# Kernel tuning notes

Measured on AMD Instinct MI355X. Metric: run time of the kernel, lower is better.

The kernel has to match this reference:

```python
import jax, jax.numpy as jnp
import numpy as np

B_, DIM, HEADS, RES = 2, 288, 12, 32
# per-branch (D_sp, H_sp, W_sp) from idx permutation of split_size=[2,2,4]
WINS = ((2, 2, 4), (2, 2, 4), (2, 4, 2))
POS_DIM = ((DIM // 3) // 4) // 4  # = 6
HB = HEADS // 3  # heads per branch = 4


def _rel_tables(Dsp, Hsp, Wsp):
    d = np.arange(1 - Dsp, Dsp); h = np.arange(1 - Hsp, Hsp); w = np.arange(1 - Wsp, Wsp)
    biases = np.stack(np.meshgrid(d, h, w, indexing='ij')).reshape(3, -1).T.astype(np.float32)
    c = np.stack(np.meshgrid(np.arange(Dsp), np.arange(Hsp), np.arange(Wsp), indexing='ij')).reshape(3, -1)
    rel = (c[:, :, None] - c[:, None, :]).transpose(1, 2, 0).astype(np.int64)
    rel[..., 0] += Dsp - 1; rel[..., 1] += Hsp - 1; rel[..., 2] += Wsp - 1
    rel[..., 0] *= (2 * Hsp - 1) * (2 * Wsp - 1); rel[..., 1] *= 2 * Wsp - 1
    return biases, rel.sum(-1).astype(np.int32)


def _ln(x, g, b):
    m = x.mean(-1, keepdims=True)
    v = jnp.mean((x - m) ** 2, axis=-1, keepdims=True)
    return (x - m) * jax.lax.rsqrt(v + 1e-5) * g + b


def setup_inputs() -> dict:
    key = jax.random.key(0)
    ks = jax.random.split(key, 10)
    C, P, L = DIM, POS_DIM, RES ** 3
    s = 0.02
    x = jax.random.normal(ks[0], (B_, L, C), jnp.float32)
    w_qkv = jax.random.normal(ks[1], (C, 3 * C), jnp.float32) * s
    w_proj = jax.random.normal(ks[2], (C, C), jnp.float32) * s
    b_proj = jnp.zeros((C,), jnp.float32)
    conv_w = jax.random.normal(ks[3], (C, 1, 3, 3, 3), jnp.float32) * s  # depthwise OIDHW
    conv_b = jnp.zeros((C,), jnp.float32)
    pos_proj_w = jax.random.normal(ks[4], (3, 3, P), jnp.float32) * s
    pos_proj_b = jnp.zeros((3, P), jnp.float32)
    ln1_g = jnp.ones((3, P)); ln1_b = jnp.zeros((3, P))
    lin1_w = jax.random.normal(ks[5], (3, P, P), jnp.float32) * s; lin1_b = jnp.zeros((3, P))
    ln2_g = jnp.ones((3, P)); ln2_b = jnp.zeros((3, P))
    lin2_w = jax.random.normal(ks[6], (3, P, P), jnp.float32) * s; lin2_b = jnp.zeros((3, P))
    ln3_g = jnp.ones((3, P)); ln3_b = jnp.zeros((3, P))
    lin3_w = jax.random.normal(ks[7], (3, P, HB), jnp.float32) * s; lin3_b = jnp.zeros((3, HB))
    tabs = [_rel_tables(*w) for w in WINS]
    rpe_biases = jnp.asarray(np.stack([t[0] for t in tabs]))  # (3, 63, 3)
    rel_index = jnp.asarray(np.stack([t[1] for t in tabs]))   # (3, 16, 16)
    return {'x': x, 'D': RES, 'H': RES, 'W': RES, 'w_qkv': w_qkv, 'w_proj': w_proj,
            'b_proj': b_proj, 'conv_w': conv_w, 'conv_b': conv_b,
            'pos_proj_w': pos_proj_w, 'pos_proj_b': pos_proj_b,
            'ln1_g': ln1_g, 'ln1_b': ln1_b, 'lin1_w': lin1_w, 'lin1_b': lin1_b,
            'ln2_g': ln2_g, 'ln2_b': ln2_b, 'lin2_w': lin2_w, 'lin2_b': lin2_b,
            'ln3_g': ln3_g, 'ln3_b': ln3_b, 'lin3_w': lin3_w, 'lin3_b': lin3_b,
            'rpe_biases': rpe_biases, 'rel_index': rel_index}


def reference(x, D, H, W, w_qkv, w_proj, b_proj, conv_w, conv_b,
              pos_proj_w, pos_proj_b, ln1_g, ln1_b, lin1_w, lin1_b,
              ln2_g, ln2_b, lin2_w, lin2_b, ln3_g, ln3_b, lin3_w, lin3_b,
              rpe_biases, rel_index):
    B, L, C = x.shape
    C3 = C // 3
    hd = C3 // HB
    scale = hd ** -0.5
    qkv = (x @ w_qkv).reshape(B, L, 3, C).transpose(2, 0, 1, 3)  # (3, B, L, C)
    outs = []
    for bi, (Dsp, Hsp, Wsp) in enumerate(WINS):
        N = Dsp * Hsp * Wsp
        lo, hi = bi * C3, (bi + 1) * C3

        def to_win(t):
            # (B, L, C3) -> windows (B', HB, N, hd)
            t = t.reshape(B, D // Dsp, Dsp, H // Hsp, Hsp, W // Wsp, Wsp, C3)
            t = t.transpose(0, 1, 3, 5, 2, 4, 6, 7).reshape(-1, N, HB, hd)
            return t.transpose(0, 2, 1, 3)

        q = to_win(qkv[0, :, :, lo:hi]) * scale
        k = to_win(qkv[1, :, :, lo:hi])
        v = to_win(qkv[2, :, :, lo:hi])
        # dynamic relative position bias MLP (residual=False path)
        p = rpe_biases[bi] @ pos_proj_w[bi] + pos_proj_b[bi]
        p = jax.nn.relu(_ln(p, ln1_g[bi], ln1_b[bi])) @ lin1_w[bi] + lin1_b[bi]
        p = jax.nn.relu(_ln(p, ln2_g[bi], ln2_b[bi])) @ lin2_w[bi] + lin2_b[bi]
        p = jax.nn.relu(_ln(p, ln3_g[bi], ln3_b[bi])) @ lin3_w[bi] + lin3_b[bi]  # (T, HB)
        bias = p[rel_index[bi].reshape(-1)].reshape(N, N, HB).transpose(2, 0, 1)  # (HB, N, N)
        attn = jax.nn.softmax(jnp.einsum('whnd,whmd->whnm', q, k) + bias[None], axis=-1)
        o = jnp.einsum('whnm,whmd->whnd', attn, v)
        o = o.transpose(0, 2, 1, 3).reshape(B, D // Dsp, H // Hsp, W // Wsp, Dsp, Hsp, Wsp, C3)
        o = o.transpose(0, 1, 4, 2, 5, 3, 6, 7).reshape(B, D, H, W, C3)
        outs.append(o)
    att = jnp.concatenate(outs, axis=-1).reshape(B, L, C)
    # locally-enhanced branch: depthwise 3x3x3 conv over v
    vimg = qkv[2].reshape(B, D, H, W, C).transpose(0, 4, 1, 2, 3)
    lcm = jax.lax.conv_general_dilated(vimg, conv_w, (1, 1, 1), 'SAME',
                                       dimension_numbers=('NCDHW', 'OIDHW', 'NCDHW'),
                                       feature_group_count=C)
    lcm = (lcm + conv_b[None, :, None, None, None]).transpose(0, 2, 3, 4, 1).reshape(B, L, C)
    return (att + lcm) @ w_proj + b_proj
```

## Files before the change

### kernel.cpp

```cpp
#include <hip/hip_runtime.h>
#include <hip/hip_bf16.h>
#include <math.h>

#define BATCH 2
#define RES   32
#define LTOK  32768
#define CDIM  288
#define NQKV  864
#define MROWS 65536

typedef unsigned short u16;
typedef u16   u16x4 __attribute__((ext_vector_type(4)));
typedef short s16x8 __attribute__((ext_vector_type(8)));
typedef float f32x4 __attribute__((ext_vector_type(4)));

__device__ __forceinline__ u16 f2bf(float f) {
  union { __hip_bfloat16 h; u16 u; } x;
  x.h = __float2bfloat16(f);
  return x.u;
}
__device__ __forceinline__ float bf2f(u16 u) {
  union { u16 u; __hip_bfloat16 h; } x;
  x.u = u;
  return __bfloat162float(x.h);
}
__device__ __forceinline__ float bflo(unsigned u) {
  union { unsigned u; float f; } x; x.u = u << 16; return x.f;
}
__device__ __forceinline__ float bfhi(unsigned u) {
  union { unsigned u; float f; } x; x.u = u & 0xffff0000u; return x.f;
}

#define ASYNC16(gsrc, ldst)                                                        \
  __builtin_amdgcn_global_load_lds(                                                \
      (const __attribute__((address_space(1))) void*)(gsrc),                       \
      (__attribute__((address_space(3))) void*)(ldst), 16, 0, 0)

__global__ __launch_bounds__(256) void transpose_cvt(
    const float* __restrict__ w, u16* __restrict__ wt, int K, int N) {
  int o = blockIdx.x * 256 + threadIdx.x;
  if (o >= N * K) return;
  int n = o / K, k = o - n * K;
  wt[o] = f2bf(w[(size_t)k * N + n]);
}

__global__ __launch_bounds__(256) void conv_w_kmajor(
    const float* __restrict__ cw, float* __restrict__ wck) {
  int o = blockIdx.x * 256 + threadIdx.x;
  if (o >= 27 * 288) return;
  int k = o / 288, c = o - k * 288;
  wck[o] = cw[c * 27 + k];
}

template <bool BF16OUT, bool ABF16>
__global__ __launch_bounds__(512, 2) void gemm_areg(
    const void* __restrict__ Ax, const u16* __restrict__ Bt,
    const float* __restrict__ bias, void* __restrict__ out, int N) {
  __shared__ __align__(16) u16 lds[36864];
  const int bm = blockIdx.x * 128;
  const int tid = threadIdx.x;
  const int lane = tid & 63, wave = tid >> 6;
  const int m16 = lane & 15, kq = lane >> 4;
  const int nf = wave >> 2, mg = wave & 3;
  const int NC = N >> 5;

  if (ABF16) {
    const u16* Ab = (const u16*)Ax;
    for (int i = wave; i < 72; i += 8) {
      int g = i >> 1, rh = i & 1;
      ASYNC16(Ab + (size_t)(bm + rh * 64 + lane) * 288 + g * 8, &lds[i * 512]);
    }
    asm volatile("s_waitcnt vmcnt(0)" ::: "memory");
  } else {
    const float* Af = (const float*)Ax;
#pragma unroll
    for (int p = 0; p < 18; p++) {
      int s = p * 512 + tid;
      int r = s / 72, q = s - r * 72;
      float4 v = *(const float4*)(Af + (size_t)(bm + r) * 288 + q * 4);
      u16x4 pk;
      pk[0] = f2bf(v.x); pk[1] = f2bf(v.y); pk[2] = f2bf(v.z); pk[3] = f2bf(v.w);
      *(u16x4*)&lds[(q >> 1) * 1024 + (r >> 6) * 512 + (r & 63) * 8 + (q & 1) * 4] = pk;
    }
  }
  __syncthreads();

  s16x8 areg[2][9];
#pragma unroll
  for (int j = 0; j < 2; j++) {
    const int row = (mg * 2 + j) * 16 + m16;
    const int base = (row >> 6) * 512 + (row & 63) * 8;
#pragma unroll
    for (int ks = 0; ks < 9; ks++)
      areg[j][ks] = *(const s16x8*)&lds[(ks * 4 + kq) * 1024 + base];
  }
  asm volatile("s_waitcnt lgkmcnt(0)" ::: "memory");
  __builtin_amdgcn_s_barrier();

  {
    const int r = lane & 31, gh = lane >> 5;
    for (int gp = wave; gp < 18; gp += 8)
      ASYNC16(Bt + (size_t)r * 288 + (gp * 2 + gh) * 8, &lds[gp * 512]);
  }
  asm volatile("s_waitcnt vmcnt(0)" ::: "memory");
  __builtin_amdgcn_s_barrier();

  int buf = 0;
  for (int c = 0; c < NC; c++) {
    if (c + 1 < NC) {
      const u16* Bc = Bt + (size_t)(c + 1) * 32 * 288;
      const int r = lane & 31, gh = lane >> 5;
      u16* bb1 = &lds[(buf ^ 1) * 9216];
      for (int gp = wave; gp < 18; gp += 8)
        ASYNC16(Bc + (size_t)r * 288 + (gp * 2 + gh) * 8, &bb1[gp * 512]);
    }
    __builtin_amdgcn_sched_barrier(0);

    const u16* bb = &lds[buf * 9216];
    f32x4 acc0 = {0.f, 0.f, 0.f, 0.f}, acc1 = {0.f, 0.f, 0.f, 0.f};
#pragma unroll
    for (int ks = 0; ks < 9; ks++) {
      s16x8 bf = *(const s16x8*)&bb[(ks * 4 + kq) * 256 + (nf * 16 + m16) * 8];
      acc0 = __builtin_amdgcn_mfma_f32_16x16x32_bf16(areg[0][ks], bf, acc0, 0, 0, 0);
      acc1 = __builtin_amdgcn_mfma_f32_16x16x32_bf16(areg[1][ks], bf, acc1, 0, 0, 0);
    }
    const int col = (c << 5) + nf * 16 + m16;
    const size_t r0 = (size_t)(bm + mg * 32 + kq * 4);
    if (BF16OUT) {
      u16* op = (u16*)out;
#pragma unroll
      for (int r = 0; r < 4; r++) {
        op[(r0 + r) * N + col] = f2bf(acc0[r]);
        op[(r0 + 16 + r) * N + col] = f2bf(acc1[r]);
      }
    } else {
      const float bv = bias ? bias[col] : 0.f;
      float* op = (float*)out;
#pragma unroll
      for (int r = 0; r < 4; r++) {
        op[(r0 + r) * N + col] = acc0[r] + bv;
        op[(r0 + 16 + r) * N + col] = acc1[r] + bv;
      }
    }
    if (c + 1 < NC) {
      asm volatile("s_waitcnt vmcnt(8)" ::: "memory");
      __builtin_amdgcn_s_barrier();
    }
    buf ^= 1;
  }
}

__device__ __forceinline__ void ln_relu6(const float* x, float* o,
                                         const float* g, const float* b) {
  float m = 0.f;
#pragma unroll
  for (int i = 0; i < 6; i++) m += x[i];
  m *= (1.f / 6.f);
  float v = 0.f;
#pragma unroll
  for (int i = 0; i < 6; i++) { float d = x[i] - m; v += d * d; }
  v *= (1.f / 6.f);
  float r = rsqrtf(v + 1e-5f);
#pragma unroll
  for (int i = 0; i < 6; i++) {
    float t = (x[i] - m) * r * g[i] + b[i];
    o[i] = t > 0.f ? t : 0.f;
  }
}

__global__ __launch_bounds__(256) void rpe_mlp(
    const float* __restrict__ rpe, const float* __restrict__ pw, const float* __restrict__ pb,
    const float* __restrict__ g1, const float* __restrict__ b1,
    const float* __restrict__ w1, const float* __restrict__ bb1,
    const float* __restrict__ g2, const float* __restrict__ b2,
    const float* __restrict__ w2, const float* __restrict__ bb2,
    const float* __restrict__ g3, const float* __restrict__ b3,
    const float* __restrict__ w3, const float* __restrict__ bb3,
    float* __restrict__ ptab) {
  int t = blockIdx.x * blockDim.x + threadIdx.x;
  if (t >= 3 * 63) return;
  int bi = t / 63, row = t % 63;
  float p[6], q[6];
#pragma unroll
  for (int j = 0; j < 6; j++) {
    float s = pb[bi * 6 + j];
#pragma unroll
    for (int i = 0; i < 3; i++) s += rpe[(bi * 63 + row) * 3 + i] * pw[(bi * 3 + i) * 6 + j];
    p[j] = s;
  }
  ln_relu6(p, q, g1 + bi * 6, b1 + bi * 6);
#pragma unroll
  for (int j = 0; j < 6; j++) {
    float s = bb1[bi * 6 + j];
#pragma unroll
    for (int i = 0; i < 6; i++) s += q[i] * w1[(bi * 6 + i) * 6 + j];
    p[j] = s;
  }
  ln_relu6(p, q, g2 + bi * 6, b2 + bi * 6);
#pragma unroll
  for (int j = 0; j < 6; j++) {
    float s = bb2[bi * 6 + j];
#pragma unroll
    for (int i = 0; i < 6; i++) s += q[i] * w2[(bi * 6 + i) * 6 + j];
    p[j] = s;
  }
  ln_relu6(p, q, g3 + bi * 6, b3 + bi * 6);
#pragma unroll
  for (int h = 0; h < 4; h++) {
    float s = bb3[bi * 4 + h];
#pragma unroll
    for (int i = 0; i < 6; i++) s += q[i] * w3[(bi * 6 + i) * 4 + h];
    ptab[(bi * 63 + row) * 4 + h] = s;
  }
}

template <bool BF16OUT>
__global__ __launch_bounds__(256) void attn_kernel(
    const u16* __restrict__ qkv, const float* __restrict__ ptab,
    const int* __restrict__ rel, float* __restrict__ y, u16* __restrict__ ybf) {
  __shared__ __align__(16) u16 sq[4][640];
  __shared__ __align__(16) u16 sk[4][640];
  __shared__ __align__(16) u16 sv[4][640];
  __shared__ __align__(16) u16 sps[4][640];

  const int bi = blockIdx.y;
  const int wsh = (bi == 2) ? 1 : 2;
  const int hsh = (bi == 2) ? 2 : 1;
  const int Wm1 = (1 << wsh) - 1, Hm1 = (1 << hsh) - 1;
  const int nW = RES >> wsh, nH = RES >> hsh;
  const int tid = threadIdx.x;
  const int wv = tid >> 6, lane = tid & 63;
  const int wid = blockIdx.x * 4 + wv;
  const int b = wid >> 11;
  const int r_ = wid & 2047;
  const int w0 = r_ % nW;
  const int r2 = r_ / nW;
  const int h0 = r2 % nH;
  const int d0 = r2 / nH;

  u16* q_  = sq[wv];
  u16* k_  = sk[wv];
  u16* v_  = sv[wv];
  u16* ps_ = sps[wv];
  const int m16 = lane & 15, q4 = lane >> 4;

  if (lane < 16) {
    uint4 z = make_uint4(0u, 0u, 0u, 0u);
    *(uint4*)&q_[lane * 40 + 24] = z;
    *(uint4*)&k_[lane * 40 + 24] = z;
    *(uint4*)&v_[lane * 40 + 24] = make_uint4(0x3f80u, 0u, 0u, 0u);
  }

  float4 pt[4];
#pragma unroll
  for (int r = 0; r < 4; r++) {
    int rv = rel[(bi * 16 + q4 * 4 + r) * 16 + m16];
    pt[r] = *(const float4*)&ptab[(size_t)(bi * 63 + rv) * 4];
  }

  size_t ybase[4];
#pragma unroll
  for (int r = 0; r < 4; r++) {
    int n = q4 * 4 + r;
    int dd = n >> 3, hh2 = (n >> wsh) & Hm1, ww = n & Wm1;
    int l = ((d0 * 2 + dd) * RES + ((h0 << hsh) + hh2)) * RES + ((w0 << wsh) + ww);
    ybase[r] = (size_t)(b * LTOK + l) * CDIM + bi * 96;
  }

  const int sn = lane / 3, sc = (lane % 3) * 8;
  size_t sbase = 0;
  if (lane < 48) {
    int dd = sn >> 3, hh2 = (sn >> wsh) & Hm1, ww = sn & Wm1;
    int l = ((d0 * 2 + dd) * RES + ((h0 << hsh) + hh2)) * RES + ((w0 << wsh) + ww);
    sbase = (size_t)(b * LTOK + l) * NQKV + bi * 96 + sc;
  }

  const float scale = 0.20412414523193154f;

  uint4 pq, pk, pv;
  if (lane < 48) {
    pq = *(const uint4*)(qkv + sbase);
    pk = *(const uint4*)(qkv + sbase + 288);
    pv = *(const uint4*)(qkv + sbase + 576);
  }

#pragma unroll
  for (int hd = 0; hd < 4; hd++) {
    if (lane < 48) {
      *(uint4*)&q_[sn * 40 + sc] = pq;
      *(uint4*)&k_[sn * 40 + sc] = pk;
      *(uint4*)&v_[sn * 40 + sc] = pv;
    }
    if (hd < 3 && lane < 48) {
      size_t nb = sbase + (size_t)(hd + 1) * 24;
      pq = *(const uint4*)(qkv + nb);
      pk = *(const uint4*)(qkv + nb + 288);
      pv = *(const uint4*)(qkv + nb + 576);
    }

    s16x8 af = *(const s16x8*)&q_[m16 * 40 + q4 * 8];
    s16x8 bf = *(const s16x8*)&k_[m16 * 40 + q4 * 8];
    f32x4 sc_ = __builtin_amdgcn_mfma_f32_16x16x32_bf16(af, bf, (f32x4){0.f, 0.f, 0.f, 0.f}, 0, 0, 0);

#pragma unroll
    for (int r = 0; r < 4; r++) {
      const float* ptr4 = (const float*)&pt[r];
      float s = sc_[r] * scale + ptr4[hd];
      float e = expf(s);
      u16 hi = f2bf(e);
      float lo = e - bf2f(hi);
      ps_[(q4 * 4 + r) * 40 + m16] = hi;
      ps_[(q4 * 4 + r) * 40 + 16 + m16] = f2bf(lo);
    }

    s16x8 pa = *(const s16x8*)&ps_[m16 * 40 + q4 * 8];
    s16x8 v1, v2;
    const int mrow = (q4 & 1) * 8;
#pragma unroll
    for (int j = 0; j < 8; j++) {
      v1[j] = (short)v_[(mrow + j) * 40 + m16];
      v2[j] = (short)v_[(mrow + j) * 40 + 16 + m16];
    }
    f32x4 o1 = __builtin_amdgcn_mfma_f32_16x16x32_bf16(pa, v1, (f32x4){0.f, 0.f, 0.f, 0.f}, 0, 0, 0);
    f32x4 o2 = __builtin_amdgcn_mfma_f32_16x16x32_bf16(pa, v2, (f32x4){0.f, 0.f, 0.f, 0.f}, 0, 0, 0);

#pragma unroll
    for (int r = 0; r < 4; r++) {
      float sum = __shfl(o2[r], (lane & 48) + 8);
      float inv = 1.f / sum;
      if (BF16OUT) {
        u16* yp = ybf + ybase[r] + hd * 24;
        yp[m16] = f2bf(o1[r] * inv);
        if (m16 < 8) yp[16 + m16] = f2bf(o2[r] * inv);
      } else {
        float* yp = y + ybase[r] + hd * 24;
        yp[m16] = o1[r] * inv;
        if (m16 < 8) yp[16 + m16] = o2[r] * inv;
      }
    }
  }
}

template <bool BF16OUT>
__global__ __launch_bounds__(512, 6) void conv_tile_kernel(
    const u16* __restrict__ qkv, const float* __restrict__ wck,
    const float* __restrict__ cb, float* __restrict__ y, u16* __restrict__ ybf) {
  __shared__ __align__(16) u16 vs[1000 * 24];
  const int tid = threadIdx.x;
  const int bx = blockIdx.x;
  const int c0 = blockIdx.y * 16;
  const int b = bx >> 6;
  const int t = bx & 63;
  const int td = (t >> 4) * 8, th = ((t >> 2) & 3) * 8, tw = (t & 3) * 8;

#pragma unroll
  for (int p = 0; p < 4; p++) {
    int idx = p * 512 + tid;
    if (idx < 2000) {
      int tok = idx >> 1, chunk = idx & 1;
      int dz = tok / 100, rem = tok - dz * 100;
      int hz = rem / 10, wz = rem - hz * 10;
      int d = td + dz - 1, h = th + hz - 1, w = tw + wz - 1;
      uint4 v = make_uint4(0u, 0u, 0u, 0u);
      if ((unsigned)d < 32u && (unsigned)h < 32u && (unsigned)w < 32u)
        v = *(const uint4*)(qkv +
              ((size_t)(b * LTOK + ((d * 32 + h) * 32 + w))) * NQKV + 576 + c0 + chunk * 8);
      *(uint4*)&vs[tok * 24 + chunk * 8] = v;
    }
  }
  __syncthreads();

  const int d = tid >> 6, h = (tid >> 3) & 7, w = tid & 7;
  float acc[16];
#pragma unroll
  for (int c = 0; c < 16; c++) acc[c] = cb[c0 + c];

  for (int kd = 0; kd < 3; kd++) {
#pragma unroll
    for (int kh = 0; kh < 3; kh++) {
#pragma unroll
      for (int kw = 0; kw < 3; kw++) {
        const int k = kd * 9 + kh * 3 + kw;
        const float* wk = wck + k * 288 + c0;
        const u16* p0 = &vs[(((d + kd) * 100 + (h + kh) * 10) + (w + kw)) * 24];
#pragma unroll
        for (int cq = 0; cq < 2; cq++) {
          uint4 v0 = *(const uint4*)(p0 + cq * 8);
          const unsigned* u0 = (const unsigned*)&v0;
#pragma unroll
          for (int j = 0; j < 4; j++) {
            const int ce = cq * 8 + j * 2;
            acc[ce]     += bflo(u0[j]) * wk[ce];
            acc[ce + 1] += bfhi(u0[j]) * wk[ce + 1];
          }
        }
      }
    }
  }

  const int tt = b * LTOK + ((td + d) * 32 + (th + h)) * 32 + (tw + w);

  if (BF16OUT) {
    uint4* yp = (uint4*)(ybf + (size_t)tt * CDIM + c0);
#pragma unroll
    for (int q = 0; q < 2; q++) {
      uint4 cur = yp[q];
      unsigned* cu = (unsigned*)&cur;
      unsigned pk2[4];
#pragma unroll
      for (int j = 0; j < 4; j++) {
        const int ce = q * 8 + j * 2;
        float a0 = bflo(cu[j]) + acc[ce];
        float a1 = bfhi(cu[j]) + acc[ce + 1];
        pk2[j] = (unsigned)f2bf(a0) | ((unsigned)f2bf(a1) << 16);
      }
      yp[q] = *(uint4*)pk2;
    }
  } else {
    float4* yp = (float4*)&y[(size_t)tt * CDIM + c0];
#pragma unroll
    for (int q = 0; q < 4; q++) {
      float4 cur = yp[q];
      cur.x += acc[q * 4];     cur.y += acc[q * 4 + 1];
      cur.z += acc[q * 4 + 2]; cur.w += acc[q * 4 + 3];
      yp[q] = cur;
    }
  }
}

extern "C" void kernel_launch(void* const* d_in, const int* in_sizes, int n_in,
                              void* d_out, int out_size, void* d_ws, size_t ws_size,
                              hipStream_t stream) {
  const float* x      = (const float*)d_in[0];
  const float* w_qkv  = (const float*)d_in[4];
  const float* w_proj = (const float*)d_in[5];
  const float* b_proj = (const float*)d_in[6];
  const float* conv_w = (const float*)d_in[7];
  const float* conv_b = (const float*)d_in[8];
  const float* pos_w  = (const float*)d_in[9];
  const float* pos_b  = (const float*)d_in[10];
  const float* ln1_g  = (const float*)d_in[11];
  const float* ln1_b  = (const float*)d_in[12];
  const float* lin1_w = (const float*)d_in[13];
  const float* lin1_b = (const float*)d_in[14];
  const float* ln2_g  = (const float*)d_in[15];
  const float* ln2_b  = (const float*)d_in[16];
  const float* lin2_w = (const float*)d_in[17];
  const float* lin2_b = (const float*)d_in[18];
  const float* ln3_g  = (const float*)d_in[19];
  const float* ln3_b  = (const float*)d_in[20];
  const float* lin3_w = (const float*)d_in[21];
  const float* lin3_b = (const float*)d_in[22];
  const float* rpe    = (const float*)d_in[23];
  const int*   rel    = (const int*)d_in[24];
  float* out = (float*)d_out;

  const size_t Q = (size_t)MROWS * NQKV * sizeof(u16);
  u16* qkv   = (u16*)d_ws;
  u16* wqt   = (u16*)((char*)d_ws + Q);
  u16* wpt   = (u16*)((char*)d_ws + Q + 497664);
  float* ptab  = (float*)((char*)d_ws + Q + 497664 + 165888);
  float* wck   = (float*)((char*)d_ws + Q + 497664 + 165888 + 3024);

  const size_t yoff = (Q + 497664 + 165888 + 3024 + 31104 + 255) & ~(size_t)255;
  const size_t ybf_bytes = (size_t)MROWS * CDIM * sizeof(u16);
  const bool big = ws_size >= yoff + ybf_bytes;
  u16* ybf = (u16*)((char*)d_ws + yoff);

  transpose_cvt<<<(NQKV * CDIM + 255) / 256, 256, 0, stream>>>(w_qkv, wqt, CDIM, NQKV);
  transpose_cvt<<<(CDIM * CDIM + 255) / 256, 256, 0, stream>>>(w_proj, wpt, CDIM, CDIM);
  conv_w_kmajor<<<(27 * 288 + 255) / 256, 256, 0, stream>>>(conv_w, wck);
  gemm_areg<true, false><<<MROWS / 128, 512, 0, stream>>>(x, wqt, nullptr, qkv, NQKV);
  rpe_mlp<<<1, 256, 0, stream>>>(rpe, pos_w, pos_b, ln1_g, ln1_b, lin1_w, lin1_b,
                                 ln2_g, ln2_b, lin2_w, lin2_b, ln3_g, ln3_b,
                                 lin3_w, lin3_b, ptab);
  if (big) {
    attn_kernel<true><<<dim3(1024, 3), 256, 0, stream>>>(qkv, ptab, rel, nullptr, ybf);
    conv_tile_kernel<true><<<dim3(128, 18), 512, 0, stream>>>(qkv, wck, conv_b, nullptr, ybf);
    gemm_areg<false, true><<<MROWS / 128, 512, 0, stream>>>(ybf, wpt, b_proj, out, CDIM);
  } else {
    attn_kernel<false><<<dim3(1024, 3), 256, 0, stream>>>(qkv, ptab, rel, out, nullptr);
    conv_tile_kernel<false><<<dim3(128, 18), 512, 0, stream>>>(qkv, wck, conv_b, out, nullptr);
    gemm_areg<false, false><<<MROWS / 128, 512, 0, stream>>>(out, wpt, b_proj, out, CDIM);
  }
}
```

Measured before the change: 342.6 us.

## Widen GEMM N-chunk to 64 columns and merge weight-prep kernels

The GEMM now processes 64 output columns per iteration instead of 32. Each wave computes a 2x2 grid of MFMA tiles, so every A register fragment feeds two B fragments, and there are half as many loop iterations and barriers. Weights are zero-padded to a multiple of 64 columns (896 and 320), with column guards on the stores, which adds some wasted MFMA work on the padding. The three weight-preparation kernels are merged into one launch to cut launch overhead.

```diff
diff --git a/kernel.cpp b/kernel.cpp
--- a/kernel.cpp
+++ b/kernel.cpp
@@ -36,20 +36,30 @@
       (const __attribute__((address_space(1))) void*)(gsrc),                       \
       (__attribute__((address_space(3))) void*)(ldst), 16, 0, 0)
 
-__global__ __launch_bounds__(256) void transpose_cvt(
-    const float* __restrict__ w, u16* __restrict__ wt, int K, int N) {
+#define WQT_ELE (896 * 288)
+#define WPT_ELE (320 * 288)
+#define WCK_ELE (27 * 288)
+__global__ __launch_bounds__(256) void prep_weights(
+    const float* __restrict__ w_qkv, const float* __restrict__ w_proj,
+    const float* __restrict__ conv_w,
+    u16* __restrict__ wqt, u16* __restrict__ wpt, float* __restrict__ wck) {
   int o = blockIdx.x * 256 + threadIdx.x;
-  if (o >= N * K) return;
-  int n = o / K, k = o - n * K;
-  wt[o] = f2bf(w[(size_t)k * N + n]);
-}
-
-__global__ __launch_bounds__(256) void conv_w_kmajor(
-    const float* __restrict__ cw, float* __restrict__ wck) {
-  int o = blockIdx.x * 256 + threadIdx.x;
-  if (o >= 27 * 288) return;
-  int k = o / 288, c = o - k * 288;
-  wck[o] = cw[c * 27 + k];
+  if (o < WQT_ELE) {
+    int n = o / 288, k = o - n * 288;
+    wqt[o] = (n < NQKV) ? f2bf(w_qkv[(size_t)k * NQKV + n]) : (u16)0;
+    return;
+  }
+  o -= WQT_ELE;
+  if (o < WPT_ELE) {
+    int n = o / 288, k = o - n * 288;
+    wpt[o] = (n < CDIM) ? f2bf(w_proj[(size_t)k * CDIM + n]) : (u16)0;
+    return;
+  }
+  o -= WPT_ELE;
+  if (o < WCK_ELE) {
+    int k = o / 288, c = o - k * 288;
+    wck[o] = conv_w[c * 27 + k];
+  }
 }
 
 template <bool BF16OUT, bool ABF16>
@@ -62,7 +72,7 @@
   const int lane = tid & 63, wave = tid >> 6;
   const int m16 = lane & 15, kq = lane >> 4;
   const int nf = wave >> 2, mg = wave & 3;
-  const int NC = N >> 5;
+  const int NCP = (N + 63) >> 6;
 
   if (ABF16) {
     const u16* Ab = (const u16*)Ax;
@@ -97,53 +107,63 @@
   asm volatile("s_waitcnt lgkmcnt(0)" ::: "memory");
   __builtin_amdgcn_s_barrier();
 
-  {
-    const int r = lane & 31, gh = lane >> 5;
-    for (int gp = wave; gp < 18; gp += 8)
-      ASYNC16(Bt + (size_t)r * 288 + (gp * 2 + gh) * 8, &lds[gp * 512]);
-  }
+  for (int gp = wave; gp < 36; gp += 8)
+    ASYNC16(Bt + (size_t)lane * 288 + gp * 8, &lds[gp * 512]);
   asm volatile("s_waitcnt vmcnt(0)" ::: "memory");
   __builtin_amdgcn_s_barrier();
 
   int buf = 0;
-  for (int c = 0; c < NC; c++) {
-    if (c + 1 < NC) {
-      const u16* Bc = Bt + (size_t)(c + 1) * 32 * 288;
-      const int r = lane & 31, gh = lane >> 5;
-      u16* bb1 = &lds[(buf ^ 1) * 9216];
-      for (int gp = wave; gp < 18; gp += 8)
-        ASYNC16(Bc + (size_t)r * 288 + (gp * 2 + gh) * 8, &bb1[gp * 512]);
+  for (int c = 0; c < NCP; c++) {
+    if (c + 1 < NCP) {
+      const u16* Bc = Bt + (size_t)(c + 1) * 64 * 288;
+      u16* bb1 = &lds[(buf ^ 1) * 18432];
+      for (int gp = wave; gp < 36; gp += 8)
+        ASYNC16(Bc + (size_t)lane * 288 + gp * 8, &bb1[gp * 512]);
     }
     __builtin_amdgcn_sched_barrier(0);
 
-    const u16* bb = &lds[buf * 9216];
-    f32x4 acc0 = {0.f, 0.f, 0.f, 0.f}, acc1 = {0.f, 0.f, 0.f, 0.f};
+    const u16* bb = &lds[buf * 18432];
+    f32x4 acc[2][2];
+#pragma unroll
+    for (int j = 0; j < 2; j++)
+#pragma unroll
+      for (int ni = 0; ni < 2; ni++) acc[j][ni] = (f32x4){0.f, 0.f, 0.f, 0.f};
+
 #pragma unroll
     for (int ks = 0; ks < 9; ks++) {
-      s16x8 bf = *(const s16x8*)&bb[(ks * 4 + kq) * 256 + (nf * 16 + m16) * 8];
-      acc0 = __builtin_amdgcn_mfma_f32_16x16x32_bf16(areg[0][ks], bf, acc0, 0, 0, 0);
-      acc1 = __builtin_amdgcn_mfma_f32_16x16x32_bf16(areg[1][ks], bf, acc1, 0, 0, 0);
-    }
-    const int col = (c << 5) + nf * 16 + m16;
+      const int g = ks * 4 + kq;
+      s16x8 bf0 = *(const s16x8*)&bb[g * 512 + (nf * 32 + m16) * 8];
+      s16x8 bf1 = *(const s16x8*)&bb[g * 512 + (nf * 32 + 16 + m16) * 8];
+      acc[0][0] = __builtin_amdgcn_mfma_f32_16x16x32_bf16(areg[0][ks], bf0, acc[0][0], 0, 0, 0);
+      acc[1][0] = __builtin_amdgcn_mfma_f32_16x16x32_bf16(areg[1][ks], bf0, acc[1][0], 0, 0, 0);
+      acc[0][1] = __builtin_amdgcn_mfma_f32_16x16x32_bf16(areg[0][ks], bf1, acc[0][1], 0, 0, 0);
+      acc[1][1] = __builtin_amdgcn_mfma_f32_16x16x32_bf16(areg[1][ks], bf1, acc[1][1], 0, 0, 0);
+    }
     const size_t r0 = (size_t)(bm + mg * 32 + kq * 4);
-    if (BF16OUT) {
-      u16* op = (u16*)out;
-#pragma unroll
-      for (int r = 0; r < 4; r++) {
-        op[(r0 + r) * N + col] = f2bf(acc0[r]);
-        op[(r0 + 16 + r) * N + col] = f2bf(acc1[r]);
+#pragma unroll
+    for (int ni = 0; ni < 2; ni++) {
+      const int col = (c << 6) + nf * 32 + ni * 16 + m16;
+      if (col < N) {
+        if (BF16OUT) {
+          u16* op = (u16*)out;
+#pragma unroll
+          for (int r = 0; r < 4; r++) {
+            op[(r0 + r) * N + col] = f2bf(acc[0][ni][r]);
+            op[(r0 + 16 + r) * N + col] = f2bf(acc[1][ni][r]);
+          }
+        } else {
+          const float bv = bias ? bias[col] : 0.f;
+          float* op = (float*)out;
+#pragma unroll
+          for (int r = 0; r < 4; r++) {
+            op[(r0 + r) * N + col] = acc[0][ni][r] + bv;
+            op[(r0 + 16 + r) * N + col] = acc[1][ni][r] + bv;
+          }
+        }
       }
-    } else {
-      const float bv = bias ? bias[col] : 0.f;
-      float* op = (float*)out;
-#pragma unroll
-      for (int r = 0; r < 4; r++) {
-        op[(r0 + r) * N + col] = acc0[r] + bv;
-        op[(r0 + 16 + r) * N + col] = acc1[r] + bv;
-      }
-    }
-    if (c + 1 < NC) {
-      asm volatile("s_waitcnt vmcnt(8)" ::: "memory");
+    }
+    if (c + 1 < NCP) {
+      asm volatile("s_waitcnt vmcnt(16)" ::: "memory");
       __builtin_amdgcn_s_barrier();
     }
     buf ^= 1;
@@ -458,18 +478,17 @@
   const size_t Q = (size_t)MROWS * NQKV * sizeof(u16);
   u16* qkv   = (u16*)d_ws;
   u16* wqt   = (u16*)((char*)d_ws + Q);
-  u16* wpt   = (u16*)((char*)d_ws + Q + 497664);
-  float* ptab  = (float*)((char*)d_ws + Q + 497664 + 165888);
-  float* wck   = (float*)((char*)d_ws + Q + 497664 + 165888 + 3024);
-
-  const size_t yoff = (Q + 497664 + 165888 + 3024 + 31104 + 255) & ~(size_t)255;
+  u16* wpt   = (u16*)((char*)d_ws + Q + 516096);
+  float* ptab  = (float*)((char*)d_ws + Q + 516096 + 184320);
+  float* wck   = (float*)((char*)d_ws + Q + 516096 + 184320 + 3024);
+
+  const size_t yoff = (Q + 516096 + 184320 + 3024 + 31104 + 255) & ~(size_t)255;
   const size_t ybf_bytes = (size_t)MROWS * CDIM * sizeof(u16);
   const bool big = ws_size >= yoff + ybf_bytes;
   u16* ybf = (u16*)((char*)d_ws + yoff);
 
-  transpose_cvt<<<(NQKV * CDIM + 255) / 256, 256, 0, stream>>>(w_qkv, wqt, CDIM, NQKV);
-  transpose_cvt<<<(CDIM * CDIM + 255) / 256, 256, 0, stream>>>(w_proj, wpt, CDIM, CDIM);
-  conv_w_kmajor<<<(27 * 288 + 255) / 256, 256, 0, stream>>>(conv_w, wck);
+  prep_weights<<<(WQT_ELE + WPT_ELE + WCK_ELE + 255) / 256, 256, 0, stream>>>(
+      w_qkv, w_proj, conv_w, wqt, wpt, wck);
   gemm_areg<true, false><<<MROWS / 128, 512, 0, stream>>>(x, wqt, nullptr, qkv, NQKV);
   rpe_mlp<<<1, 256, 0, stream>>>(rpe, pos_w, pos_b, ln1_g, ln1_b, lin1_w, lin1_b,
                                  ln2_g, ln2_b, lin2_w, lin2_b, ln3_g, ln3_b,
```

Result: no change. 347.9 us (+1.6%).
